# Performance work log

Measured on AMD Instinct MI355X. Metric: run time of the kernel, lower is better.

The kernel has to match this reference:

```python
import jax, jax.numpy as jnp
import numpy as np

NUM_NODES = 100000
NUM_EDGES = 1600000
IN_DIM = 128
OUT_DIM = 128


def setup_inputs() -> dict:
    key = jax.random.key(0)
    k_x, k_e, k_wn, k_bn, k_ws, k_bs = jax.random.split(key, 6)
    x = jax.random.normal(k_x, (NUM_NODES, IN_DIM), dtype=jnp.float32)
    edge_index = jax.random.randint(k_e, (2, NUM_EDGES), 0, NUM_NODES, dtype=jnp.int64)
    s = 1.0 / np.sqrt(IN_DIM)
    W_neigh = jax.random.uniform(k_wn, (OUT_DIM, IN_DIM), dtype=jnp.float32, minval=-s, maxval=s)
    b_neigh = jax.random.uniform(k_bn, (OUT_DIM,), dtype=jnp.float32, minval=-s, maxval=s)
    W_self = jax.random.uniform(k_ws, (OUT_DIM, IN_DIM), dtype=jnp.float32, minval=-s, maxval=s)
    b_self = jax.random.uniform(k_bs, (OUT_DIM,), dtype=jnp.float32, minval=-s, maxval=s)
    return {"x": x, "edge_index": edge_index, "W_neigh": W_neigh, "b_neigh": b_neigh,
            "W_self": W_self, "b_self": b_self}


def reference(x, edge_index, W_neigh, b_neigh, W_self, b_self):
    src, dst = edge_index[0], edge_index[1]
    # gather source node feats per edge, sum-aggregate per destination node
    msgs = x[src]  # [E, d]
    neigh = jax.ops.segment_sum(msgs, dst, num_segments=x.shape[0])  # [N, d]
    neigh_proj = neigh @ W_neigh.T + b_neigh  # [N, out]
    self_proj = x @ W_self.T + b_self         # [N, out]
    return neigh_proj + self_proj
```

## Files before the change

### kernel.cpp

```cpp
#include <hip/hip_runtime.h>
#include <hip/hip_bf16.h>

#define NN 100000
#define NE 1600000
#define DIM 128
#define BM 64
#define CAP 28
#define OVFCAP 16384
#define CVT_BLK 1024
#define SC_BLK 1024
#define CSTRIDE 4
#define XRANGE 12500

typedef __attribute__((ext_vector_type(8))) short short8;
typedef __attribute__((ext_vector_type(4))) float f32x4;
typedef __attribute__((ext_vector_type(4))) unsigned short ushort4v;

__device__ __forceinline__ unsigned short f2bf(float f) {
  union { float f; unsigned u; } v; v.f = f;
  unsigned r = v.u + 0x7fffu + ((v.u >> 16) & 1u);
  return (unsigned short)(r >> 16);
}
__device__ __forceinline__ float bf2f(unsigned short h) {
  union { unsigned u; float f; } v; v.u = ((unsigned)h) << 16;
  return v.f;
}

__global__ __launch_bounds__(256) void prep_scatter_kernel(
    const float* __restrict__ x, const int* __restrict__ ei,
    const float* __restrict__ Wn, const float* __restrict__ bn,
    const float* __restrict__ Ws, const float* __restrict__ bs,
    unsigned short* __restrict__ xb, unsigned short* __restrict__ wnb,
    unsigned short* __restrict__ wsb, float* __restrict__ bsum,
    int* __restrict__ cnt, int* __restrict__ ovfcnt, int2* __restrict__ ovf,
    int* __restrict__ slots) {
  int b = blockIdx.x;
  if (b < CVT_BLK) {
    int tid = b * 256 + threadIdx.x;
    const int stride = CVT_BLK * 256;
    const int NC = NN * DIM / 4;
    for (int i = tid; i < NC; i += stride) {
      f32x4 v = __builtin_nontemporal_load(reinterpret_cast<const f32x4*>(x) + i);
      ushort4v u;
      u[0] = f2bf(v[0]); u[1] = f2bf(v[1]); u[2] = f2bf(v[2]); u[3] = f2bf(v[3]);
      __builtin_nontemporal_store(u, reinterpret_cast<ushort4v*>(xb) + i);
    }
    if (tid < DIM * DIM) { wnb[tid] = f2bf(Wn[tid]); wsb[tid] = f2bf(Ws[tid]); }
    if (tid < DIM) bsum[tid] = bn[tid] + bs[tid];
  } else {
    const int sb  = b - CVT_BLK;
    const int lo  = (sb & 7) * XRANGE;
    const int gr  = sb >> 3;
    const int tid_g = gr * 256 + threadIdx.x;
    const int STR = 128 * 256;
    for (int e0 = tid_g; e0 < NE; e0 += 4 * STR) {
      int dj[4];
      #pragma unroll
      for (int j = 0; j < 4; ++j) {
        int ee = e0 + j * STR;
        dj[j] = (ee < NE) ? __builtin_nontemporal_load(ei + NE + ee) : -1;
      }
      #pragma unroll
      for (int j = 0; j < 4; ++j) {
        if ((unsigned)(dj[j] - lo) < (unsigned)XRANGE) {
          int ee = e0 + j * STR;
          int s = ei[ee];
          if ((unsigned)s >= NN) continue;
          int d = dj[j];
          int r = atomicAdd(&cnt[d * CSTRIDE], 1);
          if (r < CAP) {
            slots[d * CAP + r] = s;
          } else {
            int o = atomicAdd(ovfcnt, 1);
            if (o < OVFCAP) ovf[o] = make_int2(d, s);
          }
        }
      }
    }
  }
}

__global__ __launch_bounds__(512) void fusedgemm_kernel(
    const unsigned short* __restrict__ xb,
    const int* __restrict__ cnt, const int* __restrict__ slots,
    const int2* __restrict__ ovf, const int* __restrict__ ovfcnt,
    const unsigned short* __restrict__ wnb, const unsigned short* __restrict__ wsb,
    const float* __restrict__ bsum, float* __restrict__ out) {
  __shared__ unsigned short sW[DIM * DIM];
  __shared__ unsigned short sA[BM * DIM];
  __shared__ unsigned short sX[BM * DIM];
  __shared__ int2 lovf[256];
  __shared__ int lovfn;
  const int tid = threadIdx.x;
  const int row0 = blockIdx.x * BM;

  if (tid == 0) lovfn = 0;
  #pragma unroll
  for (int it = 0; it < 2; ++it) {
    int id = it * 512 + tid;
    int r = id >> 4, c = id & 15;
    int gr = row0 + r;
    short8 v = (short8)0;
    if (gr < NN) v = *reinterpret_cast<const short8*>(xb + (size_t)gr * DIM + c * 8);
    int off = (r * 256 + c * 16) ^ ((r & 7) << 4);
    *reinterpret_cast<short8*>(reinterpret_cast<char*>(sX) + off) = v;
  }
  #pragma unroll
  for (int it = 0; it < 4; ++it) {
    int id = it * 512 + tid;
    int r = id >> 4, c = id & 15;
    short8 w = *reinterpret_cast<const short8*>(wnb + r * DIM + c * 8);
    int off = (r * 256 + c * 16) ^ ((r & 7) << 4);
    *reinterpret_cast<short8*>(reinterpret_cast<char*>(sW) + off) = w;
  }
  __syncthreads();

  {
    int ovfn = min(*ovfcnt, OVFCAP);
    for (int k = tid; k < ovfn; k += 512) {
      int2 p = ovf[k];
      if ((unsigned)(p.x - row0) < (unsigned)BM) {
        int t = atomicAdd(&lovfn, 1);
        if (t < 256) lovf[t] = p;
      }
    }
  }
  __syncthreads();

  {
    const int lg = tid >> 5, ln = tid & 31;
    int g = row0 + lg;
    int m = 0, idx = 0;
    if (g < NN) {
      m = min(cnt[g * CSTRIDE], CAP);
      if (ln < m) idx = slots[g * CAP + ln];
    }
    const int lcnt = min(lovfn, 256);
    for (int it = 0; it < 4; ++it) {
      int r = it * 16 + lg;
      int gcur = row0 + r;
      int mn = 0, idxn = 0;
      if (it < 3) {
        int gn = row0 + (it + 1) * 16 + lg;
        if (gn < NN) {
          mn = min(cnt[gn * CSTRIDE], CAP);
          if (ln < mn) idxn = slots[gn * CAP + ln];
        }
      }
      f32x4 a0 = (f32x4){0.f,0.f,0.f,0.f}, a1 = a0, a2 = a0, a3 = a0;
      f32x4 a4 = a0, a5 = a0, a6 = a0, a7 = a0;
      int e = 0;
      for (; e + 7 < m; e += 8) {
        int s0 = __shfl(idx, e, 32),     s1 = __shfl(idx, e + 1, 32);
        int s2 = __shfl(idx, e + 2, 32), s3 = __shfl(idx, e + 3, 32);
        int s4 = __shfl(idx, e + 4, 32), s5 = __shfl(idx, e + 5, 32);
        int s6 = __shfl(idx, e + 6, 32), s7 = __shfl(idx, e + 7, 32);
        ushort4v u0 = *reinterpret_cast<const ushort4v*>(xb + (size_t)s0 * DIM + ln * 4);
        ushort4v u1 = *reinterpret_cast<const ushort4v*>(xb + (size_t)s1 * DIM + ln * 4);
        ushort4v u2 = *reinterpret_cast<const ushort4v*>(xb + (size_t)s2 * DIM + ln * 4);
        ushort4v u3 = *reinterpret_cast<const ushort4v*>(xb + (size_t)s3 * DIM + ln * 4);
        ushort4v u4 = *reinterpret_cast<const ushort4v*>(xb + (size_t)s4 * DIM + ln * 4);
        ushort4v u5 = *reinterpret_cast<const ushort4v*>(xb + (size_t)s5 * DIM + ln * 4);
        ushort4v u6 = *reinterpret_cast<const ushort4v*>(xb + (size_t)s6 * DIM + ln * 4);
        ushort4v u7 = *reinterpret_cast<const ushort4v*>(xb + (size_t)s7 * DIM + ln * 4);
        #pragma unroll
        for (int j = 0; j < 4; ++j) {
          a0[j] += bf2f(u0[j]); a1[j] += bf2f(u1[j]);
          a2[j] += bf2f(u2[j]); a3[j] += bf2f(u3[j]);
          a4[j] += bf2f(u4[j]); a5[j] += bf2f(u5[j]);
          a6[j] += bf2f(u6[j]); a7[j] += bf2f(u7[j]);
        }
      }
      for (; e + 3 < m; e += 4) {
        int s0 = __shfl(idx, e, 32),     s1 = __shfl(idx, e + 1, 32);
        int s2 = __shfl(idx, e + 2, 32), s3 = __shfl(idx, e + 3, 32);
        ushort4v u0 = *reinterpret_cast<const ushort4v*>(xb + (size_t)s0 * DIM + ln * 4);
        ushort4v u1 = *reinterpret_cast<const ushort4v*>(xb + (size_t)s1 * DIM + ln * 4);
        ushort4v u2 = *reinterpret_cast<const ushort4v*>(xb + (size_t)s2 * DIM + ln * 4);
        ushort4v u3 = *reinterpret_cast<const ushort4v*>(xb + (size_t)s3 * DIM + ln * 4);
        #pragma unroll
        for (int j = 0; j < 4; ++j) {
          a0[j] += bf2f(u0[j]); a1[j] += bf2f(u1[j]);
          a2[j] += bf2f(u2[j]); a3[j] += bf2f(u3[j]);
        }
      }
      for (; e < m; ++e) {
        int s0 = __shfl(idx, e, 32);
        ushort4v u0 = *reinterpret_cast<const ushort4v*>(xb + (size_t)s0 * DIM + ln * 4);
        #pragma unroll
        for (int j = 0; j < 4; ++j) a0[j] += bf2f(u0[j]);
      }
      for (int k2 = 0; k2 < lcnt; ++k2) {
        int2 p = lovf[k2];
        if (p.x == gcur) {
          ushort4v u0 = *reinterpret_cast<const ushort4v*>(xb + (size_t)p.y * DIM + ln * 4);
          #pragma unroll
          for (int j = 0; j < 4; ++j) a0[j] += bf2f(u0[j]);
        }
      }
      a0 += a1; a2 += a3; a4 += a5; a6 += a7;
      a0 += a2; a4 += a6; a0 += a4;
      ushort4v o;
      o[0] = f2bf(a0[0]); o[1] = f2bf(a0[1]); o[2] = f2bf(a0[2]); o[3] = f2bf(a0[3]);
      int off = (r * 256 + ln * 8) ^ ((r & 7) << 4);
      *reinterpret_cast<ushort4v*>(reinterpret_cast<char*>(sA) + off) = o;
      idx = idxn; m = mn;
    }
  }
  __syncthreads();

  const int wave = tid >> 6;
  const int lane = tid & 63;
  const int wm = wave & 3, wn = wave >> 2;
  const int arow = wm * 16 + (lane & 15);
  const int kl = (lane >> 4) * 8;
  f32x4 acc[4];
  #pragma unroll
  for (int t = 0; t < 4; ++t) acc[t] = (f32x4){0.f, 0.f, 0.f, 0.f};

  #pragma unroll
  for (int ks = 0; ks < 4; ++ks) {
    int k = ks * 32 + kl;
    short8 a = *reinterpret_cast<const short8*>(
        reinterpret_cast<const char*>(sA) + ((arow * 256 + k * 2) ^ ((arow & 7) << 4)));
    #pragma unroll
    for (int t = 0; t < 4; ++t) {
      int o = (wn * 4 + t) * 16 + (lane & 15);
      short8 bfr = *reinterpret_cast<const short8*>(
          reinterpret_cast<const char*>(sW) + ((o * 256 + k * 2) ^ ((o & 7) << 4)));
      acc[t] = __builtin_amdgcn_mfma_f32_16x16x32_bf16(a, bfr, acc[t], 0, 0, 0);
    }
  }
  __syncthreads();
  #pragma unroll
  for (int it = 0; it < 4; ++it) {
    int id = it * 512 + tid;
    int r = id >> 4, c = id & 15;
    short8 w = *reinterpret_cast<const short8*>(wsb + r * DIM + c * 8);
    int off = (r * 256 + c * 16) ^ ((r & 7) << 4);
    *reinterpret_cast<short8*>(reinterpret_cast<char*>(sW) + off) = w;
  }
  __syncthreads();
  #pragma unroll
  for (int ks = 0; ks < 4; ++ks) {
    int k = ks * 32 + kl;
    short8 a = *reinterpret_cast<const short8*>(
        reinterpret_cast<const char*>(sX) + ((arow * 256 + k * 2) ^ ((arow & 7) << 4)));
    #pragma unroll
    for (int t = 0; t < 4; ++t) {
      int o = (wn * 4 + t) * 16 + (lane & 15);
      short8 bfr = *reinterpret_cast<const short8*>(
          reinterpret_cast<const char*>(sW) + ((o * 256 + k * 2) ^ ((o & 7) << 4)));
      acc[t] = __builtin_amdgcn_mfma_f32_16x16x32_bf16(a, bfr, acc[t], 0, 0, 0);
    }
  }

  #pragma unroll
  for (int t = 0; t < 4; ++t) {
    int col = (wn * 4 + t) * 16 + (lane & 15);
    float bv = bsum[col];
    #pragma unroll
    for (int reg = 0; reg < 4; ++reg) {
      int gr = row0 + wm * 16 + (lane >> 4) * 4 + reg;
      if (gr < NN) out[(size_t)gr * DIM + col] = acc[t][reg] + bv;
    }
  }
}

extern "C" void kernel_launch(void* const* d_in, const int* in_sizes, int n_in,
                              void* d_out, int out_size, void* d_ws, size_t ws_size,
                              hipStream_t stream) {
  const float* x  = (const float*)d_in[0];
  const int*   ei = (const int*)d_in[1];
  const float* Wn = (const float*)d_in[2];
  const float* bn = (const float*)d_in[3];
  const float* Ws = (const float*)d_in[4];
  const float* bs = (const float*)d_in[5];
  float* out = (float*)d_out;
  char* ws = (char*)d_ws;

  unsigned short* wnb = (unsigned short*)(ws + 0);
  unsigned short* wsb = (unsigned short*)(ws + 32768);
  float* bsum        = (float*)(ws + 65536);
  int* cnt           = (int*)(ws + 66560);
  int* ovfcnt        = (int*)(ws + 1666560);
  int2* ovf          = (int2*)(ws + 1666624);
  int* slots         = (int*)(ws + 1797696);
  unsigned short* xb = (unsigned short*)(ws + 12997696);

  hipMemsetAsync(cnt, 0, 1600064, stream);
  prep_scatter_kernel<<<CVT_BLK + SC_BLK, 256, 0, stream>>>(
      x, ei, Wn, bn, Ws, bs, xb, wnb, wsb, bsum, cnt, ovfcnt, ovf, slots);
  fusedgemm_kernel<<<(NN + BM - 1) / BM, 512, 0, stream>>>(
      xb, cnt, slots, ovf, ovfcnt, wnb, wsb, bsum, out);
}
```

Baseline: 205.0 us.

## Partition node ranges into XCD-aligned slices across convert, scatter and GEMM blocks

Splits the node range into 8 slices of 12544 rows and assigns blocks by blockIdx&7 in all phases: the bf16 conversion, the edge scatter and the fused GEMM. The intent is for each XCD, assuming round-robin block dispatch, to touch only its own slice of xb, cnt and slots, so those stay in that XCD's local L2. It also drops the padded counter stride, shrinking the memset, and replaces nontemporal loads and stores with regular ones so the data stays in cache. The risk is that the scatter's counter atomics now share cache lines and contend more, and that the gathers from random source rows still cross slices.

```diff
diff --git a/kernel.cpp b/kernel.cpp
--- a/kernel.cpp
+++ b/kernel.cpp
@@ -9,8 +9,9 @@
 #define OVFCAP 16384
 #define CVT_BLK 1024
 #define SC_BLK 1024
-#define CSTRIDE 4
-#define XRANGE 12500
+#define SLICE 12544
+#define FSUB 196
+#define FGRID 1568
 
 typedef __attribute__((ext_vector_type(8))) short short8;
 typedef __attribute__((ext_vector_type(4))) float f32x4;
@@ -36,38 +37,43 @@
     int* __restrict__ slots) {
   int b = blockIdx.x;
   if (b < CVT_BLK) {
-    int tid = b * 256 + threadIdx.x;
-    const int stride = CVT_BLK * 256;
-    const int NC = NN * DIM / 4;
-    for (int i = tid; i < NC; i += stride) {
-      f32x4 v = __builtin_nontemporal_load(reinterpret_cast<const f32x4*>(x) + i);
+    const int slice = b & 7;
+    const int tid_g = (b >> 3) * 256 + threadIdx.x;
+    const int r0 = slice * SLICE;
+    const int r1 = min(r0 + SLICE, NN);
+    const int i0 = r0 * (DIM / 4), i1 = r1 * (DIM / 4);
+    for (int i = i0 + tid_g; i < i1; i += 128 * 256) {
+      f32x4 v = reinterpret_cast<const f32x4*>(x)[i];
       ushort4v u;
       u[0] = f2bf(v[0]); u[1] = f2bf(v[1]); u[2] = f2bf(v[2]); u[3] = f2bf(v[3]);
-      __builtin_nontemporal_store(u, reinterpret_cast<ushort4v*>(xb) + i);
-    }
-    if (tid < DIM * DIM) { wnb[tid] = f2bf(Wn[tid]); wsb[tid] = f2bf(Ws[tid]); }
-    if (tid < DIM) bsum[tid] = bn[tid] + bs[tid];
+      reinterpret_cast<ushort4v*>(xb)[i] = u;
+    }
+    if (slice == 0) {
+      if (tid_g < DIM * DIM) { wnb[tid_g] = f2bf(Wn[tid_g]); wsb[tid_g] = f2bf(Ws[tid_g]); }
+      if (tid_g < DIM) bsum[tid_g] = bn[tid_g] + bs[tid_g];
+    }
   } else {
     const int sb  = b - CVT_BLK;
-    const int lo  = (sb & 7) * XRANGE;
-    const int gr  = sb >> 3;
-    const int tid_g = gr * 256 + threadIdx.x;
+    const int lo  = (sb & 7) * SLICE;
+    const int hi  = min(lo + SLICE, NN);
+    const int rng = hi - lo;
+    const int tid_g = (sb >> 3) * 256 + threadIdx.x;
     const int STR = 128 * 256;
     for (int e0 = tid_g; e0 < NE; e0 += 4 * STR) {
       int dj[4];
       #pragma unroll
       for (int j = 0; j < 4; ++j) {
         int ee = e0 + j * STR;
-        dj[j] = (ee < NE) ? __builtin_nontemporal_load(ei + NE + ee) : -1;
+        dj[j] = (ee < NE) ? ei[NE + ee] : -1;
       }
       #pragma unroll
       for (int j = 0; j < 4; ++j) {
-        if ((unsigned)(dj[j] - lo) < (unsigned)XRANGE) {
+        if ((unsigned)(dj[j] - lo) < (unsigned)rng) {
           int ee = e0 + j * STR;
           int s = ei[ee];
           if ((unsigned)s >= NN) continue;
           int d = dj[j];
-          int r = atomicAdd(&cnt[d * CSTRIDE], 1);
+          int r = atomicAdd(&cnt[d], 1);
           if (r < CAP) {
             slots[d * CAP + r] = s;
           } else {
@@ -92,7 +98,8 @@
   __shared__ int2 lovf[256];
   __shared__ int lovfn;
   const int tid = threadIdx.x;
-  const int row0 = blockIdx.x * BM;
+  const int row0 = (blockIdx.x & 7) * SLICE + (blockIdx.x >> 3) * BM;
+  if (row0 >= NN) return;
 
   if (tid == 0) lovfn = 0;
   #pragma unroll
@@ -132,7 +139,7 @@
     int g = row0 + lg;
     int m = 0, idx = 0;
     if (g < NN) {
-      m = min(cnt[g * CSTRIDE], CAP);
+      m = min(cnt[g], CAP);
       if (ln < m) idx = slots[g * CAP + ln];
     }
     const int lcnt = min(lovfn, 256);
@@ -143,7 +150,7 @@
       if (it < 3) {
         int gn = row0 + (it + 1) * 16 + lg;
         if (gn < NN) {
-          mn = min(cnt[gn * CSTRIDE], CAP);
+          mn = min(cnt[gn], CAP);
           if (ln < mn) idxn = slots[gn * CAP + ln];
         }
       }
@@ -283,14 +290,14 @@
   unsigned short* wsb = (unsigned short*)(ws + 32768);
   float* bsum        = (float*)(ws + 65536);
   int* cnt           = (int*)(ws + 66560);
-  int* ovfcnt        = (int*)(ws + 1666560);
-  int2* ovf          = (int2*)(ws + 1666624);
-  int* slots         = (int*)(ws + 1797696);
-  unsigned short* xb = (unsigned short*)(ws + 12997696);
-
-  hipMemsetAsync(cnt, 0, 1600064, stream);
+  int* ovfcnt        = (int*)(ws + 466560);
+  int2* ovf          = (int2*)(ws + 466688);
+  int* slots         = (int*)(ws + 597760);
+  unsigned short* xb = (unsigned short*)(ws + 11797760);
+
+  hipMemsetAsync(cnt, 0, 400064, stream);
   prep_scatter_kernel<<<CVT_BLK + SC_BLK, 256, 0, stream>>>(
       x, ei, Wn, bn, Ws, bs, xb, wnb, wsb, bsum, cnt, ovfcnt, ovf, slots);
-  fusedgemm_kernel<<<(NN + BM - 1) / BM, 512, 0, stream>>>(
+  fusedgemm_kernel<<<FGRID, 512, 0, stream>>>(
       xb, cnt, slots, ovf, ovfcnt, wnb, wsb, bsum, out);
 }
```

After: 179.7 us. 12.4% less time.
